# Performance work log

Measured on AMD Instinct MI355X. Metric: run time of the kernel, lower is better.

The kernel has to match this reference:

```python
import jax, jax.numpy as jnp
from jax import lax
import numpy as np

B, N, C = 8, 10647, 80          # batch, total anchors (416px YOLOv3), COCO classes
MAX_BOXES = 100                  # yolo_max_boxes (per class and total, like combined NMS)
IOU_TH = 0.5
SCORE_TH = 0.3


def setup_inputs() -> dict:
    key = jax.random.key(0)
    k1, k2, k3, k4 = jax.random.split(key, 4)
    # valid corner-format boxes (x1,y1,x2,y2) in [0,1]
    xy = jax.random.uniform(k1, (B, N, 2), dtype=jnp.float32) * 0.9
    wh = jax.random.uniform(k2, (B, N, 2), dtype=jnp.float32) * 0.1 + 0.01
    boxes = jnp.concatenate([xy, xy + wh], axis=-1)
    confidence = jax.random.uniform(k3, (B, N, 1), dtype=jnp.float32)
    class_probs = jax.random.uniform(k4, (B, N, C), dtype=jnp.float32)
    return {"boxes": boxes, "confidence": confidence, "class_probs": class_probs}


def _iou_one_vs_all(box, boxes):
    # box [4], boxes [N,4], corner format
    x1 = jnp.maximum(box[0], boxes[:, 0])
    y1 = jnp.maximum(box[1], boxes[:, 1])
    x2 = jnp.minimum(box[2], boxes[:, 2])
    y2 = jnp.minimum(box[3], boxes[:, 3])
    inter = jnp.maximum(x2 - x1, 0.0) * jnp.maximum(y2 - y1, 0.0)
    area_a = (box[2] - box[0]) * (box[3] - box[1])
    area_b = (boxes[:, 2] - boxes[:, 0]) * (boxes[:, 3] - boxes[:, 1])
    return inter / (area_a + area_b - inter + 1e-9)


def _nms_one_class(scores_c, bxs):
    # scores_c [N], bxs [N,4]: greedy NMS, returns MAX_BOXES candidates
    s0 = jnp.where(scores_c > SCORE_TH, scores_c, -1.0)

    def step(cur, _):
        i = jnp.argmax(cur)
        sc = cur[i]
        b = bxs[i]
        ious = _iou_one_vs_all(b, bxs)
        nxt = jnp.where(ious > IOU_TH, -1.0, cur).at[i].set(-1.0)
        valid = sc > 0.0
        return nxt, (jnp.where(valid, sc, 0.0),
                     jnp.where(valid, b, jnp.zeros(4, b.dtype)),
                     valid)

    _, (ss, bb, vv) = lax.scan(step, s0, None, length=MAX_BOXES)
    return bb, ss, vv  # [M,4], [M], [M]


def reference(boxes, confidence, class_probs):
    # scores per class: objectness * class prob  -> [B, C, N]
    scores = jnp.transpose(confidence * class_probs, (0, 2, 1))
    per_class = jax.vmap(jax.vmap(_nms_one_class, in_axes=(0, None)), in_axes=(0, 0))
    cb, cs, cv = per_class(scores, boxes)           # [B,C,M,4], [B,C,M], [B,C,M]

    flat_s = cs.reshape(B, -1)                       # [B, C*M]
    flat_b = cb.reshape(B, -1, 4)
    flat_v = cv.reshape(B, -1)
    cls_ids = jnp.broadcast_to(
        jnp.arange(C, dtype=jnp.float32)[:, None], (C, MAX_BOXES)).reshape(-1)

    top_s, top_i = lax.top_k(flat_s, MAX_BOXES)      # merge across classes
    sel_b = jnp.take_along_axis(flat_b, top_i[..., None], axis=1)
    sel_v = jnp.take_along_axis(flat_v, top_i, axis=1)
    sel_c = jnp.where(sel_v, cls_ids[top_i], 0.0)
    sel_s = jnp.where(sel_v, top_s, 0.0)
    num_valid = jnp.sum(sel_v, axis=1).astype(jnp.int32)
    return sel_b, sel_s, sel_c, num_valid
```

## Files before the change

### kernel.cpp

```cpp
#include <hip/hip_runtime.h>

#define Bn 8
#define Nn 10647
#define Cn 80
#define MAXB 100
#define SCORE_TH 0.3f
#define BGUESS 0.82f
#define IOU_THR 0.5f
#define NBIN 4096
#define NB2 1024
#define SORT_CAP 256
#define TARGET 160
#define CH 128
#define PCAP 16
#define TOT (Cn * MAXB)
#define TOTQ (TOT / 4)
#define MREG 8

__device__ __forceinline__ int score_bin(float s) {
    int v = (int)(__float_as_uint(s) >> 12) - 0x3E999 + 1;
    v = v < 1 ? 1 : v;
    return v > NBIN - 1 ? NBIN - 1 : v;
}
__device__ __forceinline__ int score_bin2(float s) {
    int v = (int)(__float_as_uint(s) >> 14) - 0xFA66 + 1;
    v = v < 1 ? 1 : v;
    return v > NB2 - 1 ? NB2 - 1 : v;
}

__device__ __forceinline__ bool iou_gt(const float4 s, const float4 c) {
    float x1 = fmaxf(s.x, c.x), y1 = fmaxf(s.y, c.y);
    float x2 = fminf(s.z, c.z), y2 = fminf(s.w, c.w);
    float inter = fmaxf(x2 - x1, 0.0f) * fmaxf(y2 - y1, 0.0f);
    float aS = (s.z - s.x) * (s.w - s.y);
    float aC = (c.z - c.x) * (c.w - c.y);
    return inter > IOU_THR * (aS + aC - inter + 1e-9f);
}

__global__ __launch_bounds__(256) void collect(
    const float* __restrict__ conf, const float* __restrict__ cp,
    const float4* __restrict__ boxes,
    int* __restrict__ pcnt, unsigned long long* __restrict__ gkey,
    float4* __restrict__ gbox)
{
    __shared__ float lconf[88];
    __shared__ int cnt3[Cn];
    __shared__ int cnt9[Cn];
    int tid = threadIdx.x;
    int b = blockIdx.x / CH;
    int ch = blockIdx.x % CH;

    for (int i = tid; i < Cn; i += 256) { cnt3[i] = 0; cnt9[i] = 0; }

    const int totq = Nn * 20;
    const int per = (totq + CH - 1) / CH;
    int q0 = ch * per;
    int q1 = q0 + per; if (q1 > totq) q1 = totq;
    int n0 = q0 / 20;
    int nspan = (q1 - 1) / 20 - n0 + 1;

    const float* confB = conf + b * Nn;
    for (int i = tid; i < nspan; i += 256) lconf[i] = confB[n0 + i];
    __syncthreads();

    const float4* cp4 = (const float4*)(cp + (size_t)b * Nn * Cn);
    const float4* boxesB = boxes + (size_t)b * Nn;

    for (int q = q0 + tid; q < q1; q += 512) {
        int qb = q + 256;
        bool has2 = qb < q1;
        float4 v1 = cp4[q];
        float4 v2 = has2 ? cp4[qb] : make_float4(0, 0, 0, 0);
#pragma unroll
        for (int h = 0; h < 2; ++h) {
            if (h == 1 && !has2) break;
            int qq = (h == 0) ? q : qb;
            float4 v = (h == 0) ? v1 : v2;
            int n = qq / 20;
            int c0 = (qq % 20) * 4;
            float cf = lconf[n - n0];
            float sv[4] = {v.x, v.y, v.z, v.w};
#pragma unroll
            for (int e = 0; e < 4; ++e) {
                float s = cf * sv[e];
                if (s > SCORE_TH) {
                    atomicAdd(&cnt3[c0 + e], 1);
                    if (s > BGUESS) {
                        int pos = atomicAdd(&cnt9[c0 + e], 1);
                        if (pos < PCAP) {
                            size_t idx = ((size_t)(b * Cn + c0 + e) * CH + ch) * PCAP + pos;
                            gkey[idx] = ((unsigned long long)__float_as_uint(s) << 32) |
                                        (unsigned)(Nn - 1 - n);
                            gbox[idx] = boxesB[n];
                        }
                    }
                }
            }
        }
    }
    __syncthreads();
    for (int c = tid; c < Cn; c += 256)
        pcnt[(size_t)(b * Cn + c) * CH + ch] = (cnt3[c] & 0xFFFF) | (cnt9[c] << 16);
}

__global__ __launch_bounds__(512) void nms_class(
    const float4* __restrict__ boxes, const float* __restrict__ conf,
    const float* __restrict__ cp,
    const int* __restrict__ pcnt, const unsigned long long* __restrict__ gkey,
    const float4* __restrict__ gbox,
    float* __restrict__ wss, float4* __restrict__ wsb)
{
    __shared__ unsigned long long keys[SORT_CAP];
    __shared__ float4 bxc[SORT_CAP];
    __shared__ float ssc[SORT_CAP];
    __shared__ float4 sbx[SORT_CAP];
    __shared__ float4 bxu[SORT_CAP];
    __shared__ unsigned short cj[SORT_CAP][3];
    __shared__ int ncA[SORT_CAP];
    __shared__ unsigned char selv[SORT_CAP], resv[SORT_CAP], confl[SORT_CAP];
    __shared__ int rpart[SORT_CAP];
    __shared__ int chc[CH], chOff[CH], pscan[CH];
    __shared__ int hist2[NB2];
    __shared__ int suf[257];
    __shared__ int wtot[4];
    __shared__ int sh_ovf, sh_hard, sh_B, sh_M, sh_nsel;

    int tid = threadIdx.x;
    int lane = tid & 63, wv = tid >> 6;
    int bc = blockIdx.x;
    int b = bc / Cn, c = bc % Cn;

    if (tid == 0) { sh_ovf = 0; sh_hard = 0; sh_nsel = 0; }
    for (int i = tid; i < SORT_CAP; i += 512) ncA[i] = 0;
    __syncthreads();

    if (tid < CH) {
        int p = pcnt[(size_t)(b * Cn + c) * CH + tid];
        int c9 = p >> 16;
        if (c9 > PCAP) { atomicOr(&sh_ovf, 1); c9 = PCAP; }
        chc[tid] = c9;
        int incl = c9;
#pragma unroll
        for (int off = 1; off < 64; off <<= 1) {
            int o = __shfl_up(incl, off);
            if (lane >= off) incl += o;
        }
        pscan[tid] = incl;
        int t3 = p & 0xFFFF;
#pragma unroll
        for (int off = 32; off > 0; off >>= 1) t3 += __shfl_down(t3, off);
        if (lane == 0) wtot[wv] = t3;
    }
    float* ws_s = wss + bc * MAXB;
    float4* ws_b = wsb + bc * MAXB;
    for (int i = tid; i < MAXB; i += 512) ws_s[i] = 0.0f;
    __syncthreads();
    if (tid < CH) {
        int base = (tid >= 64) ? pscan[63] : 0;
        chOff[tid] = base + pscan[tid] - chc[tid];
    }
    __syncthreads();

    int cnt = pscan[63] + pscan[127];
    int tot = wtot[0] + wtot[1];
    bool fast = (!sh_ovf) && (cnt <= SORT_CAP);
    int M = fast ? cnt : 0;

    if (fast) {
        size_t base = (size_t)(b * Cn + c) * CH * PCAP;
        for (int i = tid; i < CH * PCAP; i += 512) {
            int ch = i >> 4, j = i & (PCAP - 1);
            if (j < chc[ch]) {
                int dst = chOff[ch] + j;
                keys[dst] = gkey[base + i];
                bxc[dst] = gbox[base + i];
            }
        }
    }
    __syncthreads();

    int cand = tid & 255, half = tid >> 8;
    bool act = (cand < M);

    unsigned long long k0 = 0;
    float4 b0 = make_float4(0, 0, 0, 0);
    if (act) k0 = keys[cand];
    if (act && half == 0) b0 = bxc[cand];
    int r0 = 0;
    if (act) {
#pragma unroll 4
        for (int j = half; j < M; j += 2) r0 += (keys[j] > k0) ? 1 : 0;
    }
    if (act && half == 1) rpart[cand] = r0;
    __syncthreads();
    if (act && half == 0) {
        int rank = r0 + rpart[cand];
        ssc[rank] = __uint_as_float((unsigned)(k0 >> 32));
        sbx[rank] = b0;
    }
    __syncthreads();

    if (act) {
        float4 tb = sbx[cand];
#pragma unroll 4
        for (int j = half; j < cand; j += 2) {
            float4 bj = sbx[j];
            if (iou_gt(bj, tb)) {
                int s = atomicAdd(&ncA[cand], 1);
                if (s < 3) cj[cand][s] = (unsigned short)j;
            }
        }
    }
    __syncthreads();
    if (tid < SORT_CAP && tid < M && ncA[tid] > 3) atomicOr(&sh_hard, 1);
    __syncthreads();

    if (!sh_hard) {
        bool mysel = false, myres = false;
        if (tid < SORT_CAP) {
            myres = (tid < M) ? (ncA[tid] == 0) : true;
            mysel = (tid < M) && myres;
            selv[tid] = mysel ? 1 : 0;
            resv[tid] = myres ? 1 : 0;
        }
        __syncthreads();
        while (true) {
            bool upd = false, upd_sel = false;
            if (tid < SORT_CAP && tid < M && !myres) {
                int nc = ncA[tid];
                bool allr = true, anysel = false;
                for (int k = 0; k < nc; ++k) {
                    int j = cj[tid][k];
                    allr = allr && (resv[j] != 0);
                    anysel = anysel || (selv[j] != 0);
                }
                if (allr) { upd = true; upd_sel = !anysel; }
            }
            __syncthreads();
            if (upd) {
                myres = true; mysel = upd_sel;
                selv[tid] = mysel ? 1 : 0; resv[tid] = 1;
            }
            int unres = __syncthreads_count((tid < SORT_CAP && tid < M && !myres) ? 1 : 0);
            if (unres == 0) break;
        }
        int v = (tid < SORT_CAP && mysel) ? 1 : 0;
        int incl = v;
        if (tid < SORT_CAP) {
#pragma unroll
            for (int off = 1; off < 64; off <<= 1) {
                int o = __shfl_up(incl, off);
                if (lane >= off) incl += o;
            }
            if (lane == 63) wtot[wv] = incl;
        }
        __syncthreads();
        if (tid < SORT_CAP) {
            int base = 0;
            for (int w = 0; w < wv; ++w) base += wtot[w];
            int pos = base + incl - v;
            if (v && pos < MAXB) { ws_s[pos] = ssc[tid]; ws_b[pos] = sbx[tid]; }
            if (tid == 0) sh_nsel = wtot[0] + wtot[1] + wtot[2] + wtot[3];
        }
        __syncthreads();
    } else {
        if (tid < SORT_CAP) confl[tid] = (tid < M && ncA[tid] > 0) ? 1 : 0;
        __syncthreads();
        if (tid < 64) {
            float4 sA = make_float4(0, 0, 0, 0), sB = make_float4(0, 0, 0, 0);
            int nsel = 0;
            for (int w0 = 0; w0 < M && nsel < MAXB; w0 += 64) {
                int wlim = M - w0; if (wlim > 64) wlim = 64;
                bool cfl = (tid < wlim) ? (confl[w0 + tid] != 0) : false;
                unsigned long long cmask = __ballot(cfl);
                int pos = 0;
                while (pos < wlim && nsel < MAXB) {
                    if (!((cmask >> pos) & 1ULL)) {
                        unsigned long long rest = cmask >> pos;
                        int run = rest ? (__ffsll(rest) - 1) : (wlim - pos);
                        if (run > wlim - pos) run = wlim - pos;
                        int avail = MAXB - nsel; if (run > avail) run = avail;
                        int d = (tid - (nsel & 63)) & 63;
                        if (d < run) {
                            int s = nsel + d;
                            int ci = w0 + pos + d;
                            float4 bx = sbx[ci];
                            if (s < 64) sA = bx; else sB = bx;
                            ws_s[s] = ssc[ci]; ws_b[s] = bx;
                        }
                        nsel += run; pos += run;
                    } else {
                        int ci = w0 + pos;
                        float4 bx = sbx[ci];
                        bool sup = (tid < nsel) && iou_gt(sA, bx);
                        if (tid + 64 < nsel) sup = sup || iou_gt(sB, bx);
                        if (__ballot(sup) == 0ULL) {
                            if (tid == (nsel & 63)) { if (nsel < 64) sA = bx; else sB = bx; }
                            if (tid == 0) { ws_s[nsel] = ssc[ci]; ws_b[nsel] = bx; }
                            ++nsel;
                        }
                        ++pos;
                    }
                }
            }
            if (tid == 0) sh_nsel = nsel;
        }
        __syncthreads();
    }

    bool needSlow = (!fast) || !((sh_nsel >= MAXB) || (cnt == tot));
    if (!needSlow) return;

    for (int i = tid; i < MAXB; i += 512) ws_s[i] = 0.0f;
    for (int i = tid; i < NB2; i += 512) hist2[i] = 0;
    if (tid == 0) sh_nsel = 0;
    __syncthreads();

    const float4* boxesB = boxes + (size_t)b * Nn;
    const float* confB = conf + b * Nn;
    const float* cpB = cp + (size_t)b * Nn * Cn + c;
    for (int n = tid; n < Nn; n += 512) {
        float s = confB[n] * cpB[(size_t)n * Cn];
        if (s > SCORE_TH) atomicAdd(&hist2[score_bin2(s)], 1);
    }
    __syncthreads();

    float4 sA = make_float4(0, 0, 0, 0), sB = make_float4(0, 0, 0, 0);
    int hi = NB2;
    int round = 0;

    while (true) {
        if (tid < 256) {
            int ps = 0;
#pragma unroll
            for (int u = 0; u < 4; ++u) ps += hist2[tid * 4 + u];
            int p = ps;
#pragma unroll
            for (int off = 1; off < 64; off <<= 1) {
                int v = __shfl_down(p, off);
                if (lane + off < 64) p += v;
            }
            if (lane == 0) wtot[wv] = p;
            pscan[0] = p;
            suf[tid] = p;
        }
        __syncthreads();
        if (tid < 256) {
            int add = 0;
            for (int w2 = wv + 1; w2 < 4; ++w2) add += wtot[w2];
            suf[tid] = suf[tid] + add;
            if (tid == 0) suf[256] = 0;
        }
        __syncthreads();

        int total = suf[0];
        if (total == 0) break;

        int target = total < TARGET ? total : TARGET;
        if (tid < 256 && suf[tid] >= target && suf[tid + 1] < target) sh_B = tid;
        if (tid == 0) sh_M = 0;
        __syncthreads();
        if (tid == 0) {
            int g = sh_B;
            int running = suf[g + 1];
            int B = g * 4;
            for (int u = 3; u >= 0; --u) {
                running += hist2[g * 4 + u];
                if (running >= target) { B = g * 4 + u; break; }
            }
            sh_B = B;
        }
        __syncthreads();
        int B = sh_B;

        for (int n = tid; n < Nn; n += 512) {
            float s = confB[n] * cpB[(size_t)n * Cn];
            if (s > SCORE_TH) {
                int bin = score_bin2(s);
                if (bin >= B && bin < hi) {
                    int pos2 = atomicAdd(&sh_M, 1);
                    if (pos2 < SORT_CAP)
                        keys[pos2] = ((unsigned long long)__float_as_uint(s) << 32) |
                                     (unsigned)(Nn - 1 - n);
                }
            }
        }
        __syncthreads();
        int M2 = sh_M; if (M2 > SORT_CAP) M2 = SORT_CAP;

        unsigned long long mk = 0;
        float4 mb = make_float4(0, 0, 0, 0);
        if (tid < 256) {
            if (tid < M2) { mk = keys[tid]; mb = boxesB[Nn - 1 - (int)(mk & 0xffffffffu)]; }
            bxu[tid] = mb;
        }
        __syncthreads();

        if (tid < 256) {
            int rank = 0;
            bool cfl = (round > 0);
            for (int j = 0; j < M2; ++j) {
                unsigned long long kk = keys[j];
                float4 bj = bxu[j];
                bool gt = kk > mk;
                rank += gt ? 1 : 0;
                if (round == 0) cfl = cfl || (gt && iou_gt(bj, mb));
            }
            if (tid < M2) {
                ssc[rank] = __uint_as_float((unsigned)(mk >> 32));
                sbx[rank] = mb; confl[rank] = cfl ? 1 : 0;
            }
        }
        __syncthreads();

        if (tid < 64) {
            int nsel = sh_nsel;
            for (int w0 = 0; w0 < M2 && nsel < MAXB; w0 += 64) {
                int wlim = M2 - w0; if (wlim > 64) wlim = 64;
                bool cfl2 = (tid < wlim) ? (confl[w0 + tid] != 0) : false;
                unsigned long long cmask = __ballot(cfl2);
                int pos = 0;
                while (pos < wlim && nsel < MAXB) {
                    if (!((cmask >> pos) & 1ULL)) {
                        unsigned long long rest = cmask >> pos;
                        int run = rest ? (__ffsll(rest) - 1) : (wlim - pos);
                        if (run > wlim - pos) run = wlim - pos;
                        int avail = MAXB - nsel; if (run > avail) run = avail;
                        int d = (tid - (nsel & 63)) & 63;
                        if (d < run) {
                            int s = nsel + d;
                            int ci = w0 + pos + d;
                            float4 bx = sbx[ci];
                            if (s < 64) sA = bx; else sB = bx;
                            ws_s[s] = ssc[ci]; ws_b[s] = bx;
                        }
                        nsel += run; pos += run;
                    } else {
                        int ci = w0 + pos;
                        float4 bx = sbx[ci];
                        bool sup = (tid < nsel) && iou_gt(sA, bx);
                        if (tid + 64 < nsel) sup = sup || iou_gt(sB, bx);
                        if (__ballot(sup) == 0ULL) {
                            if (tid == (nsel & 63)) { if (nsel < 64) sA = bx; else sB = bx; }
                            if (tid == 0) { ws_s[nsel] = ssc[ci]; ws_b[nsel] = bx; }
                            ++nsel;
                        }
                        ++pos;
                    }
                }
            }
            if (tid == 0) sh_nsel = nsel;
        }
        __syncthreads();
        if (sh_nsel >= MAXB) break;
        for (int i = B + tid; i < NB2; i += 512) hist2[i] = 0;
        hi = B;
        ++round;
        __syncthreads();
    }
}

__global__ __launch_bounds__(256) void merge_topk(
    const float* __restrict__ wss, const float4* __restrict__ wsb,
    float* __restrict__ out)
{
    __shared__ int hist[NBIN];
    __shared__ int suf[257];
    __shared__ int wtot[4];
    __shared__ unsigned long long keys[SORT_CAP];
    __shared__ unsigned long long skeys[SORT_CAP];
    __shared__ int sh_B, sh_M;

    int tid = threadIdx.x, b = blockIdx.x;
    int lane = tid & 63, wv = tid >> 6;
    for (int i = tid; i < NBIN / 4; i += 256) ((int4*)hist)[i] = make_int4(0, 0, 0, 0);
    if (tid == 0) sh_M = 0;
    skeys[tid] = 0ULL;
    __syncthreads();

    const float4* w4 = (const float4*)(wss + b * TOT);
    float4 rr[MREG];
#pragma unroll
    for (int k = 0; k < MREG; ++k) {
        int q = tid + k * 256;
        rr[k] = (q < TOTQ) ? w4[q] : make_float4(0, 0, 0, 0);
    }
#pragma unroll
    for (int k = 0; k < MREG; ++k) {
        float4 v = rr[k];
        if (v.x > 0.0f) atomicAdd(&hist[score_bin(v.x)], 1);
        if (v.y > 0.0f) atomicAdd(&hist[score_bin(v.y)], 1);
        if (v.z > 0.0f) atomicAdd(&hist[score_bin(v.z)], 1);
        if (v.w > 0.0f) atomicAdd(&hist[score_bin(v.w)], 1);
    }
    __syncthreads();

    int ps = 0;
#pragma unroll
    for (int u = 0; u < 16; ++u) ps += hist[tid * 16 + u];
    int p = ps;
#pragma unroll
    for (int off = 1; off < 64; off <<= 1) {
        int v = __shfl_down(p, off);
        if (lane + off < 64) p += v;
    }
    if (lane == 0) wtot[wv] = p;
    __syncthreads();
    int add = 0;
    for (int w2 = wv + 1; w2 < 4; ++w2) add += wtot[w2];
    suf[tid] = p + add;
    if (tid == 0) suf[256] = 0;
    __syncthreads();

    int total = suf[0];
    int target = total < MAXB ? total : MAXB;

    if (total > 0) {
        if (suf[tid] >= target && suf[tid + 1] < target) sh_B = tid;
    }
    __syncthreads();
    if (total > 0 && tid == 0) {
        int g = sh_B;
        int running = suf[g + 1];
        int B = g * 16;
        for (int u = 15; u >= 0; --u) {
            running += hist[g * 16 + u];
            if (running >= target) { B = g * 16 + u; break; }
        }
        sh_B = B;
    }
    __syncthreads();
    if (total > 0) {
        int B = sh_B;
#pragma unroll
        for (int k = 0; k < MREG; ++k) {
            int q = tid + k * 256;
            if (q < TOTQ) {
                float4 v = rr[k];
                int ib = q * 4;
                float sv[4] = {v.x, v.y, v.z, v.w};
#pragma unroll
                for (int e = 0; e < 4; ++e) {
                    float s = sv[e];
                    if (s > 0.0f && score_bin(s) >= B) {
                        int pos = atomicAdd(&sh_M, 1);
                        if (pos < SORT_CAP)
                            keys[pos] = ((unsigned long long)__float_as_uint(s) << 32) |
                                        (unsigned)(TOT - 1 - (ib + e));
                    }
                }
            }
        }
    }
    __syncthreads();
    int M = sh_M; if (M > SORT_CAP) M = SORT_CAP;

    unsigned long long mykey = (tid < M) ? keys[tid] : 0ULL;
    int rank = 0;
    for (int j = 0; j < M; ++j) rank += (keys[j] > mykey) ? 1 : 0;
    if (tid < M) skeys[rank] = mykey;
    __syncthreads();

    bool valid = false;
    if (tid < MAXB) {
        unsigned long long g = skeys[tid];
        valid = (g != 0ULL);
        float s = valid ? __uint_as_float((unsigned)(g >> 32)) : 0.0f;
        int f = TOT - 1 - (int)(g & 0xffffffffu);
        float4 bx = make_float4(0, 0, 0, 0);
        float cls = 0.0f;
        if (valid) { bx = wsb[b * TOT + f]; cls = (float)(f / MAXB); }
        ((float4*)out)[b * MAXB + tid] = bx;
        out[Bn * MAXB * 4 + b * MAXB + tid] = s;
        out[Bn * MAXB * 5 + b * MAXB + tid] = cls;
    }
    int nv = __syncthreads_count(valid);
    if (tid == 0) out[Bn * MAXB * 6 + b] = (float)nv;
}

extern "C" void kernel_launch(void* const* d_in, const int* in_sizes, int n_in,
                              void* d_out, int out_size, void* d_ws, size_t ws_size,
                              hipStream_t stream) {
    const float4* boxes = (const float4*)d_in[0];
    const float* conf   = (const float*)d_in[1];
    const float* cp     = (const float*)d_in[2];
    float* out = (float*)d_out;

    char* ws = (char*)d_ws;
    int* pcnt = (int*)(ws + 0);
    unsigned long long* gkey = (unsigned long long*)(ws + 327680);
    float4* gbox = (float4*)(ws + 10813440);
    float* wss = (float*)(ws + 31784960);
    float4* wsb = (float4*)(ws + 32040960);

    collect<<<Bn * CH, 256, 0, stream>>>(conf, cp, boxes, pcnt, gkey, gbox);
    nms_class<<<Bn * Cn, 512, 0, stream>>>(boxes, conf, cp, pcnt, gkey, gbox,
                                           wss, wsb);
    merge_topk<<<Bn, 256, 0, stream>>>(wss, wsb, out);
}
```

Before: 53.65 us.

## Drop box copies from collect; gather boxes by index in NMS with prefetch

The collect kernel no longer writes candidate boxes to a workspace buffer. It stores only packed score and index keys, and its loop goes from two elements per thread to one. The NMS kernel now loads all 2048 key slots unconditionally at entry, before the first barrier, and gathers boxes from the input by decoded index so that the loads overlap the count and scan setup. The fixed-point resolution loop is also capped at three rounds, falling back to the conflict path otherwise. The trade-off is that the kernel reads key slots that may hold stale data, guarded by clamping the index, and spends more registers.

```diff
diff --git a/kernel.cpp b/kernel.cpp
--- a/kernel.cpp
+++ b/kernel.cpp
@@ -39,9 +39,7 @@
 
 __global__ __launch_bounds__(256) void collect(
     const float* __restrict__ conf, const float* __restrict__ cp,
-    const float4* __restrict__ boxes,
-    int* __restrict__ pcnt, unsigned long long* __restrict__ gkey,
-    float4* __restrict__ gbox)
+    int* __restrict__ pcnt, unsigned long long* __restrict__ glist)
 {
     __shared__ float lconf[88];
     __shared__ int cnt3[Cn];
@@ -64,36 +62,24 @@
     __syncthreads();
 
     const float4* cp4 = (const float4*)(cp + (size_t)b * Nn * Cn);
-    const float4* boxesB = boxes + (size_t)b * Nn;
-
-    for (int q = q0 + tid; q < q1; q += 512) {
-        int qb = q + 256;
-        bool has2 = qb < q1;
-        float4 v1 = cp4[q];
-        float4 v2 = has2 ? cp4[qb] : make_float4(0, 0, 0, 0);
-#pragma unroll
-        for (int h = 0; h < 2; ++h) {
-            if (h == 1 && !has2) break;
-            int qq = (h == 0) ? q : qb;
-            float4 v = (h == 0) ? v1 : v2;
-            int n = qq / 20;
-            int c0 = (qq % 20) * 4;
-            float cf = lconf[n - n0];
-            float sv[4] = {v.x, v.y, v.z, v.w};
-#pragma unroll
-            for (int e = 0; e < 4; ++e) {
-                float s = cf * sv[e];
-                if (s > SCORE_TH) {
-                    atomicAdd(&cnt3[c0 + e], 1);
-                    if (s > BGUESS) {
-                        int pos = atomicAdd(&cnt9[c0 + e], 1);
-                        if (pos < PCAP) {
-                            size_t idx = ((size_t)(b * Cn + c0 + e) * CH + ch) * PCAP + pos;
-                            gkey[idx] = ((unsigned long long)__float_as_uint(s) << 32) |
-                                        (unsigned)(Nn - 1 - n);
-                            gbox[idx] = boxesB[n];
-                        }
-                    }
+
+    for (int q = q0 + tid; q < q1; q += 256) {
+        float4 v = cp4[q];
+        int n = q / 20;
+        int c0 = (q % 20) * 4;
+        float cf = lconf[n - n0];
+        float sv[4] = {v.x, v.y, v.z, v.w};
+#pragma unroll
+        for (int e = 0; e < 4; ++e) {
+            float s = cf * sv[e];
+            if (s > SCORE_TH) {
+                atomicAdd(&cnt3[c0 + e], 1);
+                if (s > BGUESS) {
+                    int pos = atomicAdd(&cnt9[c0 + e], 1);
+                    if (pos < PCAP)
+                        glist[((size_t)(b * Cn + c0 + e) * CH + ch) * PCAP + pos] =
+                            ((unsigned long long)__float_as_uint(s) << 32) |
+                            (unsigned)(Nn - 1 - n);
                 }
             }
         }
@@ -107,7 +93,6 @@
     const float4* __restrict__ boxes, const float* __restrict__ conf,
     const float* __restrict__ cp,
     const int* __restrict__ pcnt, const unsigned long long* __restrict__ gkey,
-    const float4* __restrict__ gbox,
     float* __restrict__ wss, float4* __restrict__ wsb)
 {
     __shared__ unsigned long long keys[SORT_CAP];
@@ -130,9 +115,22 @@
     int bc = blockIdx.x;
     int b = bc / Cn, c = bc % Cn;
 
+    const float4* boxesB = boxes + (size_t)b * Nn;
+
+    size_t base = (size_t)(b * Cn + c) * CH * PCAP;
+    unsigned long long sv[4];
+    float4 bv[4];
+#pragma unroll
+    for (int k = 0; k < 4; ++k) sv[k] = gkey[base + tid + k * 512];
+#pragma unroll
+    for (int k = 0; k < 4; ++k) {
+        int n = Nn - 1 - (int)(sv[k] & 0xffffffffu);
+        n = n < 0 ? 0 : (n > Nn - 1 ? Nn - 1 : n);
+        bv[k] = boxesB[n];
+    }
+
     if (tid == 0) { sh_ovf = 0; sh_hard = 0; sh_nsel = 0; }
     for (int i = tid; i < SORT_CAP; i += 512) ncA[i] = 0;
-    __syncthreads();
 
     if (tid < CH) {
         int p = pcnt[(size_t)(b * Cn + c) * CH + tid];
@@ -156,8 +154,8 @@
     for (int i = tid; i < MAXB; i += 512) ws_s[i] = 0.0f;
     __syncthreads();
     if (tid < CH) {
-        int base = (tid >= 64) ? pscan[63] : 0;
-        chOff[tid] = base + pscan[tid] - chc[tid];
+        int base2 = (tid >= 64) ? pscan[63] : 0;
+        chOff[tid] = base2 + pscan[tid] - chc[tid];
     }
     __syncthreads();
 
@@ -167,13 +165,14 @@
     int M = fast ? cnt : 0;
 
     if (fast) {
-        size_t base = (size_t)(b * Cn + c) * CH * PCAP;
-        for (int i = tid; i < CH * PCAP; i += 512) {
+#pragma unroll
+        for (int k = 0; k < 4; ++k) {
+            int i = tid + k * 512;
             int ch = i >> 4, j = i & (PCAP - 1);
             if (j < chc[ch]) {
                 int dst = chOff[ch] + j;
-                keys[dst] = gkey[base + i];
-                bxc[dst] = gbox[base + i];
+                keys[dst] = sv[k];
+                bxc[dst] = bv[k];
             }
         }
     }
@@ -215,6 +214,7 @@
     if (tid < SORT_CAP && tid < M && ncA[tid] > 3) atomicOr(&sh_hard, 1);
     __syncthreads();
 
+    bool fastResolved = false;
     if (!sh_hard) {
         bool mysel = false, myres = false;
         if (tid < SORT_CAP) {
@@ -224,7 +224,8 @@
             resv[tid] = myres ? 1 : 0;
         }
         __syncthreads();
-        while (true) {
+        int unres = 1;
+        for (int rr = 0; rr < 3 && unres; ++rr) {
             bool upd = false, upd_sel = false;
             if (tid < SORT_CAP && tid < M && !myres) {
                 int nc = ncA[tid];
@@ -241,29 +242,34 @@
                 myres = true; mysel = upd_sel;
                 selv[tid] = mysel ? 1 : 0; resv[tid] = 1;
             }
-            int unres = __syncthreads_count((tid < SORT_CAP && tid < M && !myres) ? 1 : 0);
-            if (unres == 0) break;
-        }
-        int v = (tid < SORT_CAP && mysel) ? 1 : 0;
-        int incl = v;
-        if (tid < SORT_CAP) {
-#pragma unroll
-            for (int off = 1; off < 64; off <<= 1) {
-                int o = __shfl_up(incl, off);
-                if (lane >= off) incl += o;
-            }
-            if (lane == 63) wtot[wv] = incl;
-        }
-        __syncthreads();
-        if (tid < SORT_CAP) {
-            int base = 0;
-            for (int w = 0; w < wv; ++w) base += wtot[w];
-            int pos = base + incl - v;
-            if (v && pos < MAXB) { ws_s[pos] = ssc[tid]; ws_b[pos] = sbx[tid]; }
-            if (tid == 0) sh_nsel = wtot[0] + wtot[1] + wtot[2] + wtot[3];
-        }
-        __syncthreads();
-    } else {
+            unres = __syncthreads_count((tid < SORT_CAP && tid < M && !myres) ? 1 : 0);
+        }
+        if (unres == 0) {
+            fastResolved = true;
+            int v = (tid < SORT_CAP && mysel) ? 1 : 0;
+            int incl = v;
+            if (tid < SORT_CAP) {
+#pragma unroll
+                for (int off = 1; off < 64; off <<= 1) {
+                    int o = __shfl_up(incl, off);
+                    if (lane >= off) incl += o;
+                }
+                if (lane == 63) wtot[wv] = incl;
+            }
+            __syncthreads();
+            if (tid < SORT_CAP) {
+                int base2 = 0;
+                for (int w = 0; w < wv; ++w) base2 += wtot[w];
+                int pos = base2 + incl - v;
+                if (v && pos < MAXB) { ws_s[pos] = ssc[tid]; ws_b[pos] = sbx[tid]; }
+                if (tid == 0) sh_nsel = wtot[0] + wtot[1] + wtot[2] + wtot[3];
+            }
+            __syncthreads();
+        }
+    }
+
+    if (!fastResolved) {
+        for (int i = tid; i < MAXB; i += 512) ws_s[i] = 0.0f;
         if (tid < SORT_CAP) confl[tid] = (tid < M && ncA[tid] > 0) ? 1 : 0;
         __syncthreads();
         if (tid < 64) {
@@ -316,7 +322,6 @@
     if (tid == 0) sh_nsel = 0;
     __syncthreads();
 
-    const float4* boxesB = boxes + (size_t)b * Nn;
     const float* confB = conf + b * Nn;
     const float* cpB = cp + (size_t)b * Nn * Cn + c;
     for (int n = tid; n < Nn; n += 512) {
@@ -341,7 +346,6 @@
                 if (lane + off < 64) p += v;
             }
             if (lane == 0) wtot[wv] = p;
-            pscan[0] = p;
             suf[tid] = p;
         }
         __syncthreads();
@@ -589,12 +593,10 @@
     char* ws = (char*)d_ws;
     int* pcnt = (int*)(ws + 0);
     unsigned long long* gkey = (unsigned long long*)(ws + 327680);
-    float4* gbox = (float4*)(ws + 10813440);
-    float* wss = (float*)(ws + 31784960);
-    float4* wsb = (float4*)(ws + 32040960);
-
-    collect<<<Bn * CH, 256, 0, stream>>>(conf, cp, boxes, pcnt, gkey, gbox);
-    nms_class<<<Bn * Cn, 512, 0, stream>>>(boxes, conf, cp, pcnt, gkey, gbox,
-                                           wss, wsb);
+    float* wss = (float*)(ws + 10813440);
+    float4* wsb = (float4*)(ws + 11069440);
+
+    collect<<<Bn * CH, 256, 0, stream>>>(conf, cp, pcnt, gkey);
+    nms_class<<<Bn * Cn, 512, 0, stream>>>(boxes, conf, cp, pcnt, gkey, wss, wsb);
     merge_topk<<<Bn, 256, 0, stream>>>(wss, wsb, out);
 }
```

Result: no change. 54.72 us (+2.0%).
